# Performance work log

Hardware: AMD Instinct MI355X
Metric: run time of the kernel (lower is better)

## Reference

```python
import jax, jax.numpy as jnp
import numpy as np

NUM_HEADS = 16
THETA = 10000.0


def _rope(x, pos, theta):
    # x: [b, h, s, d_k] with d_k even; rotate interleaved pairs (even, odd)
    d = x.shape[-1]
    inv_freq = theta ** (-jnp.arange(0, d, 2, dtype=jnp.float32) / d)  # [d/2]
    ang = pos.astype(jnp.float32)[:, None] * inv_freq                  # [s, d/2]
    cos = jnp.cos(ang)[None, None]                                     # [1,1,s,d/2]
    sin = jnp.sin(ang)[None, None]
    x1 = x[..., 0::2]
    x2 = x[..., 1::2]
    r1 = x1 * cos - x2 * sin
    r2 = x1 * sin + x2 * cos
    return jnp.stack([r1, r2], axis=-1).reshape(x.shape)


def setup_inputs() -> dict:
    key = jax.random.key(0)
    ks = jax.random.split(key, 5)
    B, S, D = 2, 2048, 1024
    x = jax.random.normal(ks[0], (B, S, D), dtype=jnp.float32)
    scale = 0.02
    Wq = jax.random.normal(ks[1], (D, D), dtype=jnp.float32) * scale
    Wk = jax.random.normal(ks[2], (D, D), dtype=jnp.float32) * scale
    Wv = jax.random.normal(ks[3], (D, D), dtype=jnp.float32) * scale
    Wo = jax.random.normal(ks[4], (D, D), dtype=jnp.float32) * scale
    return {"x": x, "Wq": Wq, "Wk": Wk, "Wv": Wv, "Wo": Wo}


def reference(x, Wq, Wk, Wv, Wo):
    B, S, D = x.shape
    H = NUM_HEADS
    dk = D // H
    # QKV projections (bias-free Linear: y = x @ W^T, W is [out, in])
    q = (x @ Wq.T).reshape(B, S, H, dk).transpose(0, 2, 1, 3)  # [b,h,s,dk]
    k = (x @ Wk.T).reshape(B, S, H, dk).transpose(0, 2, 1, 3)
    v = (x @ Wv.T).reshape(B, S, H, dk).transpose(0, 2, 1, 3)
    pos = jnp.arange(S)
    q = _rope(q, pos, THETA)
    k = _rope(k, pos, THETA)
    # naive masked SDPA, causal mask
    scores = jnp.einsum('bhqd,bhkd->bhqk', q, k) / (dk ** 0.5)
    causal = jnp.tril(jnp.ones((S, S), dtype=bool))
    scores = jnp.where(causal, scores, -jnp.inf)
    attn = jax.nn.softmax(scores, axis=-1)
    out = jnp.einsum('bhqk,bhkd->bhqd', attn, v)
    out = out.transpose(0, 2, 1, 3).reshape(B, S, D)
    return out @ Wo.T
```

## Files before the change

### kernel.cpp

```cpp
#include <hip/hip_runtime.h>
#include <hip/hip_bf16.h>
#include <stdint.h>

typedef __bf16 bf16;
typedef __bf16 bf16x8 __attribute__((ext_vector_type(8)));
typedef float f32x4 __attribute__((ext_vector_type(4)));
typedef float f32x16 __attribute__((ext_vector_type(16)));

#define B_ 2
#define S_ 2048
#define D_ 1024
#define H_ 16
#define DK 64
#define M_ 4096

__device__ __forceinline__ void gload_lds16(const void* g, void* l) {
  __builtin_amdgcn_global_load_lds(
      (const __attribute__((address_space(1))) uint32_t*)(uintptr_t)g,
      (__attribute__((address_space(3))) uint32_t*)(uintptr_t)l, 16, 0, 0);
}

__device__ __forceinline__ uint32_t pkbf(float a, float b) {
  union { uint32_t u; struct { bf16 x, y; } s; } r;
  r.s.x = (bf16)a; r.s.y = (bf16)b;
  return r.u;
}

struct alignas(8) B4s { bf16 a, b, c, d; };

__global__ __launch_bounds__(256) void cvt_all_kernel(
    const float* __restrict__ x, const float* __restrict__ wq, const float* __restrict__ wk,
    const float* __restrict__ wv, const float* __restrict__ wo,
    bf16* __restrict__ xb, bf16* __restrict__ wqb, bf16* __restrict__ wkb,
    bf16* __restrict__ wvb, bf16* __restrict__ wob) {
  int i = blockIdx.x * 256 + threadIdx.x;
  const float* src;
  bf16* dst;
  int off;
  if (i < 1048576) { src = x; dst = xb; off = i; }
  else if (i < 1310720) { src = wq; dst = wqb; off = i - 1048576; }
  else if (i < 1572864) { src = wk; dst = wkb; off = i - 1310720; }
  else if (i < 1835008) { src = wv; dst = wvb; off = i - 1572864; }
  else { src = wo; dst = wob; off = i - 1835008; }
  float4 v = reinterpret_cast<const float4*>(src)[off];
  B4s o{(bf16)v.x, (bf16)v.y, (bf16)v.z, (bf16)v.w};
  reinterpret_cast<B4s*>(dst)[off] = o;
}

template <int MODE>
__global__ __launch_bounds__(256, 3) void gemm_kernel(
    const bf16* __restrict__ A,
    const bf16* __restrict__ W0, const bf16* __restrict__ W1, const bf16* __restrict__ W2,
    bf16* __restrict__ q_out, bf16* __restrict__ k_out, bf16* __restrict__ v_out,
    float* __restrict__ c_out) {
  constexpr int BK = 64;
  constexpr int BM = (MODE == 0) ? 128 : 64;
  constexpr int BNR = (MODE == 0) ? 128 : 64;
  constexpr int AM = (MODE == 0) ? 2 : 1;
  constexpr int BN = (MODE == 0) ? 2 : 1;
  constexpr int NT = (MODE == 0) ? 24 : 16;
  constexpr int PERX = (MODE == 0) ? 96 : 128;
  __shared__ bf16 Alds[BM * BK];
  __shared__ bf16 Blds[BNR * BK];
  const int tid = threadIdx.x;
  const int w = tid >> 6, l = tid & 63;
  const int l31 = l & 31, hh = l >> 5;
  const int lin = (blockIdx.x & 7) * PERX + (blockIdx.x >> 3);
  const int m0 = (lin / NT) * BM;
  const int nt = lin % NT;
  const bf16* W;
  int n0;
  const int rt = (MODE == 0) ? (nt >> 3) : 0;
  if (MODE == 0) {
    W = rt == 0 ? W0 : (rt == 1 ? W1 : W2);
    n0 = (nt & 7) * 128;
  } else {
    W = W0;
    n0 = nt * 64;
  }
  const int K = 1024;
  const int wm = (MODE == 0) ? (w >> 1) * 64 : (w & 1) * 32;
  const int wn = (MODE == 0) ? (w & 1) * 64 : (w >> 1) * 32;
  const int srow = w * 8 + (l >> 3);
  const int scol = ((l & 7) * 8) ^ (((l >> 3) & 7) * 8);
  const int swz = (l & 7) * 8;
  f32x16 acc[AM][BN] = {};
  for (int k0 = 0; k0 < K; k0 += BK) {
    const bf16* Ab = A + (size_t)m0 * K + k0;
    const bf16* Bb = W + (size_t)n0 * K + k0;
#pragma unroll
    for (int c = 0; c < BM / 32; ++c)
      gload_lds16(Ab + (size_t)(c * 32 + srow) * K + scol, Alds + (c * 32 + w * 8) * BK);
#pragma unroll
    for (int c = 0; c < BNR / 32; ++c)
      gload_lds16(Bb + (size_t)(c * 32 + srow) * K + scol, Blds + (c * 32 + w * 8) * BK);
    __syncthreads();
    bf16x8 af[AM][4], bfr[BN][4];
#pragma unroll
    for (int am = 0; am < AM; ++am)
#pragma unroll
      for (int t = 0; t < 4; ++t)
        af[am][t] = *reinterpret_cast<const bf16x8*>(
            Alds + (wm + am * 32 + l31) * BK + ((t * 16 + hh * 8) ^ swz));
#pragma unroll
    for (int bn = 0; bn < BN; ++bn)
#pragma unroll
      for (int t = 0; t < 4; ++t)
        bfr[bn][t] = *reinterpret_cast<const bf16x8*>(
            Blds + (wn + bn * 32 + l31) * BK + ((t * 16 + hh * 8) ^ swz));
#pragma unroll
    for (int t = 0; t < 4; ++t)
#pragma unroll
      for (int am = 0; am < AM; ++am)
#pragma unroll
        for (int bn = 0; bn < BN; ++bn)
          acc[am][bn] = __builtin_amdgcn_mfma_f32_32x32x16_bf16(af[am][t], bfr[bn][t],
                                                               acc[am][bn], 0, 0, 0);
    __syncthreads();
  }
#pragma unroll
  for (int am = 0; am < AM; ++am)
#pragma unroll
    for (int bn = 0; bn < BN; ++bn)
#pragma unroll
      for (int r = 0; r < 16; ++r) {
        int m = m0 + wm + am * 32 + (r & 3) + 8 * (r >> 2) + 4 * hh;
        int n = n0 + wn + bn * 32 + l31;
        float v = acc[am][bn][r];
        if (MODE == 0) {
          bf16* dst = rt == 0 ? q_out : (rt == 1 ? k_out : v_out);
          int h = n >> 6, d = n & 63;
          int b = m >> 11, s = m & 2047;
          dst[(((size_t)b * H_ + h) * S_ + s) * DK + d] = (bf16)v;
        } else {
          c_out[(size_t)m * D_ + n] = v;
        }
      }
}

__global__ __launch_bounds__(256) void rope_kernel(bf16* __restrict__ Q, bf16* __restrict__ K) {
  const int NG = 32 * 2048 * 8;
  int idx = blockIdx.x * 256 + threadIdx.x;
  bf16* X = Q;
  float sc = 0.18033688f;
  if (idx >= NG) { X = K; idx -= NG; sc = 1.0f; }
  int g = idx & 7;
  int s = (idx >> 3) & 2047;
  int bh = idx >> 14;
  size_t off = ((size_t)bh * S_ + s) * DK + g * 8;
  bf16x8 v = *reinterpret_cast<const bf16x8*>(X + off);
  bf16x8 o;
  const float c0 = -0.4152410118609203f;
  float fs = (float)s;
#pragma unroll
  for (int p = 0; p < 4; ++p) {
    int i = g * 4 + p;
    float ang = fs * exp2f((float)i * c0);
    float sn = __sinf(ang), cs = __cosf(ang);
    float x1 = (float)v[2 * p], x2 = (float)v[2 * p + 1];
    o[2 * p]     = (bf16)((x1 * cs - x2 * sn) * sc);
    o[2 * p + 1] = (bf16)((x1 * sn + x2 * cs) * sc);
  }
  *reinterpret_cast<bf16x8*>(X + off) = o;
}

__global__ __launch_bounds__(256, 4) void attn_kernel(
    const bf16* __restrict__ Q, const bf16* __restrict__ K, const bf16* __restrict__ V,
    bf16* __restrict__ O) {
  __shared__ __align__(16) char smem[40960];
  bf16* K3 = (bf16*)smem;
  bf16* Vt2 = (bf16*)smem + 12288;
  float* MG = (float*)smem;
  const int tid = threadIdx.x;
  const int w = tid >> 6, l = tid & 63;
  const int ql = l & 31, h = l >> 5;
  const int kh = w >> 1, qh = w & 1;
  const int bid = blockIdx.x;
  const int u = (bid >> 5) & 7;
  const int j = bid >> 8;
  const int qt = (j == 0) ? u : (j == 1) ? 31 - u : (j == 2) ? u + 8 : 23 - u;
  const int bh = bid & 31;
  const size_t base = (size_t)bh * S_ * DK;

  const size_t qrow = base + (size_t)(qt * 64 + qh * 32 + ql) * DK;
  bf16x8 qf[4];
#pragma unroll
  for (int t = 0; t < 4; ++t)
    qf[t] = *reinterpret_cast<const bf16x8*>(Q + qrow + t * 16 + h * 8);

  float l_run = 0.f;
  f32x16 o0 = {}, o1 = {};

  auto stageK = [&](int kt, int buf) {
#pragma unroll
    for (int c = 0; c < 2; ++c) {
      int row = c * 32 + w * 8 + (l >> 3);
      int col = ((l & 7) * 8) ^ ((row & 7) * 8);
      gload_lds16(K + base + (size_t)(kt * 64 + row) * DK + col,
                  K3 + buf * 4096 + c * 2048 + w * 512);
    }
  };
  auto loadV = [&](int kt, bf16x8 (&pv)[2]) {
    const bf16* vp = V + base + (size_t)(kt * 64 + l) * DK + w * 16;
    pv[0] = *reinterpret_cast<const bf16x8*>(vp);
    pv[1] = *reinterpret_cast<const bf16x8*>(vp + 8);
  };
  auto writeV = [&](int vb, const bf16x8 (&pv)[2]) {
    bf16* Vt = Vt2 + vb * 4096;
#pragma unroll
    for (int j2 = 0; j2 < 8; ++j2) {
      Vt[(w * 16 + j2) * 64 + (l ^ (j2 * 8))] = pv[0][j2];
      Vt[(w * 16 + 8 + j2) * 64 + (l ^ (j2 * 8))] = pv[1][j2];
    }
  };

  {
    bf16x8 pv[2];
    loadV(0, pv);
    stageK(0, 0);
    if (qt >= 1) stageK(1, 1);
    writeV(0, pv);
    if (qt >= 1) {
      asm volatile("s_waitcnt vmcnt(2)" ::: "memory");
    } else {
      asm volatile("s_waitcnt vmcnt(0)" ::: "memory");
    }
    asm volatile("s_waitcnt lgkmcnt(0)" ::: "memory");
    __builtin_amdgcn_sched_barrier(0);
    __builtin_amdgcn_s_barrier();
    __builtin_amdgcn_sched_barrier(0);
  }

  const int swzd = (ql & 7) * 8;
  const int keyA = kh * 32 + ql;
  const int limq = qh * 32 + ql;
  bf16x8 pvv[2];
  int kb = 0, kb2 = 2;

  for (int kt = 0; kt <= qt; ++kt) {
    const int vb = kt & 1;
    const bool pre = kt < qt;
    const bool pre2 = kt + 2 <= qt;
    const bool lastt = (kt == qt);
    const bool skipw = lastt && (kh == 1) && (qh == 0);
    if (pre) loadV(kt + 1, pvv);
    if (pre2) stageK(kt + 2, kb2);
    if (!skipw) {
      f32x16 ss = {};
      __builtin_amdgcn_s_setprio(1);
#pragma unroll
      for (int t = 0; t < 4; ++t) {
        bf16x8 kf = *reinterpret_cast<const bf16x8*>(
            K3 + kb * 4096 + keyA * 64 + ((t * 16 + h * 8) ^ ((keyA & 7) * 8)));
        ss = __builtin_amdgcn_mfma_f32_32x32x16_bf16(kf, qf[t], ss, 0, 0, 0);
      }
      __builtin_amdgcn_s_setprio(0);
      if (lastt) {
#pragma unroll
        for (int r = 0; r < 16; ++r) {
          int kl = kh * 32 + (r & 3) + 8 * (r >> 2) + 4 * h;
          if (kl > limq) ss[r] = -INFINITY;
        }
      }
      float t0 = 0.f, t1 = 0.f, t2 = 0.f, t3 = 0.f;
#pragma unroll
      for (int r = 0; r < 16; r += 4) {
        float p0 = exp2f(ss[r]);
        float p1 = exp2f(ss[r + 1]);
        float p2 = exp2f(ss[r + 2]);
        float p3 = exp2f(ss[r + 3]);
        ss[r] = p0; ss[r + 1] = p1; ss[r + 2] = p2; ss[r + 3] = p3;
        t0 += p0; t1 += p1; t2 += p2; t3 += p3;
      }
      l_run += (t0 + t1) + (t2 + t3);
      uint32_t Wq_[4][2];
#pragma unroll
      for (int g = 0; g < 4; ++g) {
        Wq_[g][0] = pkbf(ss[4 * g + 0], ss[4 * g + 1]);
        Wq_[g][1] = pkbf(ss[4 * g + 2], ss[4 * g + 3]);
      }
      __builtin_amdgcn_s_setprio(1);
#pragma unroll
      for (int ks = 0; ks < 2; ++ks) {
        uint32_t a0 = Wq_[2 * ks][0], a1 = Wq_[2 * ks][1];
        uint32_t b0 = Wq_[2 * ks + 1][0], b1 = Wq_[2 * ks + 1][1];
        uint32_t sxa0 = (uint32_t)__shfl_xor((int)a0, 32);
        uint32_t sxa1 = (uint32_t)__shfl_xor((int)a1, 32);
        uint32_t sxb0 = (uint32_t)__shfl_xor((int)b0, 32);
        uint32_t sxb1 = (uint32_t)__shfl_xor((int)b1, 32);
        union { uint32_t u[4]; bf16x8 v; } pa;
        pa.u[0] = h ? sxb0 : a0;
        pa.u[1] = h ? sxb1 : a1;
        pa.u[2] = h ? b0 : sxa0;
        pa.u[3] = h ? b1 : sxa1;
        int col = (kh * 32 + ks * 16 + h * 8) ^ swzd;
        const bf16* Vt = Vt2 + vb * 4096;
        bf16x8 v0 = *reinterpret_cast<const bf16x8*>(&Vt[ql * 64 + col]);
        bf16x8 v1 = *reinterpret_cast<const bf16x8*>(&Vt[(32 + ql) * 64 + col]);
        o0 = __builtin_amdgcn_mfma_f32_32x32x16_bf16(pa.v, v0, o0, 0, 0, 0);
        o1 = __builtin_amdgcn_mfma_f32_32x32x16_bf16(pa.v, v1, o1, 0, 0, 0);
      }
      __builtin_amdgcn_s_setprio(0);
    }
    if (pre) writeV(vb ^ 1, pvv);
    asm volatile("s_waitcnt vmcnt(2)" ::: "memory");
    asm volatile("s_waitcnt lgkmcnt(0)" ::: "memory");
    __builtin_amdgcn_sched_barrier(0);
    __builtin_amdgcn_s_barrier();
    __builtin_amdgcn_sched_barrier(0);
    kb = (kb == 2) ? 0 : kb + 1;
    kb2 = (kb2 == 2) ? 0 : kb2 + 1;
  }

  l_run += __shfl_xor(l_run, 32);
  __syncthreads();
  if (kh == 1) {
    int off = (qh * 64 + l) * 33;
    MG[off] = l_run;
#pragma unroll
    for (int r = 0; r < 16; ++r) {
      MG[off + 1 + r] = o0[r];
      MG[off + 17 + r] = o1[r];
    }
  }
  __syncthreads();
  if (kh == 0) {
    int off = (qh * 64 + l) * 33;
    float inv = 1.0f / (l_run + MG[off]);
    const int b = bh >> 4, hd = bh & 15;
#pragma unroll
    for (int r = 0; r < 16; ++r) {
      int rowl = (r & 3) + 8 * (r >> 2) + 4 * h;
      float invr = __shfl(inv, rowl);
      int qr = qt * 64 + qh * 32 + rowl;
      size_t ooff = ((size_t)b * S_ + qr) * D_ + hd * 64;
      O[ooff + ql] = (bf16)((o0[r] + MG[off + 1 + r]) * invr);
      O[ooff + 32 + ql] = (bf16)((o1[r] + MG[off + 17 + r]) * invr);
    }
  }
}

extern "C" void kernel_launch(void* const* d_in, const int* in_sizes, int n_in,
                              void* d_out, int out_size, void* d_ws, size_t ws_size,
                              hipStream_t stream) {
  const float* x  = (const float*)d_in[0];
  const float* Wq = (const float*)d_in[1];
  const float* Wk = (const float*)d_in[2];
  const float* Wv = (const float*)d_in[3];
  const float* Wo = (const float*)d_in[4];
  float* out = (float*)d_out;
  char* ws = (char*)d_ws;

  bf16* xb  = (bf16*)(ws + ((size_t)0 << 20));
  bf16* wqb = (bf16*)(ws + ((size_t)8 << 20));
  bf16* wkb = (bf16*)(ws + ((size_t)10 << 20));
  bf16* wvb = (bf16*)(ws + ((size_t)12 << 20));
  bf16* wob = (bf16*)(ws + ((size_t)14 << 20));
  bf16* Qb  = (bf16*)(ws + ((size_t)16 << 20));
  bf16* Kb  = (bf16*)(ws + ((size_t)24 << 20));
  bf16* Vb  = (bf16*)(ws + ((size_t)32 << 20));
  bf16* Ob  = (bf16*)(ws + ((size_t)40 << 20));

  cvt_all_kernel<<<8192, 256, 0, stream>>>(x, Wq, Wk, Wv, Wo, xb, wqb, wkb, wvb, wob);
  gemm_kernel<0><<<768, 256, 0, stream>>>(xb, wqb, wkb, wvb, Qb, Kb, Vb, nullptr);
  rope_kernel<<<4096, 256, 0, stream>>>(Qb, Kb);
  attn_kernel<<<1024, 256, 0, stream>>>(Qb, Kb, Vb, Ob);
  gemm_kernel<1><<<1024, 256, 0, stream>>>(Ob, wob, nullptr, nullptr, nullptr, nullptr,
                                           nullptr, out);
}
```

Baseline: 105.2 us.

## Triple-buffer GEMM LDS staging with BK=32 and async prefetch two tiles ahead

Restructures the projection GEMM main loop from a single-buffered load-sync-compute pattern into a three-stage LDS ring that prefetches tiles two k-steps ahead using global_load_lds. Manual vmcnt waits and a single barrier per step replace the two __syncthreads. The K tile is halved to 32 to keep LDS use bounded, with a matching new swizzle. The goal is to hide global memory latency behind MFMA work, at the cost of more loop iterations and hand-written waitcnt logic that must be exactly right.

```diff
diff --git a/kernel.cpp b/kernel.cpp
--- a/kernel.cpp
+++ b/kernel.cpp
@@ -53,15 +53,21 @@
     const bf16* __restrict__ W0, const bf16* __restrict__ W1, const bf16* __restrict__ W2,
     bf16* __restrict__ q_out, bf16* __restrict__ k_out, bf16* __restrict__ v_out,
     float* __restrict__ c_out) {
-  constexpr int BK = 64;
+  constexpr int BK = 32;
   constexpr int BM = (MODE == 0) ? 128 : 64;
   constexpr int BNR = (MODE == 0) ? 128 : 64;
   constexpr int AM = (MODE == 0) ? 2 : 1;
   constexpr int BN = (MODE == 0) ? 2 : 1;
   constexpr int NT = (MODE == 0) ? 24 : 16;
   constexpr int PERX = (MODE == 0) ? 96 : 128;
-  __shared__ bf16 Alds[BM * BK];
-  __shared__ bf16 Blds[BNR * BK];
+  constexpr int AE = BM * BK;
+  constexpr int BE = BNR * BK;
+  constexpr int ACALLS = BM / 64;
+  constexpr int BCALLS = BNR / 64;
+  constexpr int INF = ACALLS + BCALLS;
+  __shared__ bf16 smem[3 * (AE + BE)];
+  bf16* Ab3 = smem;
+  bf16* Bb3 = smem + 3 * AE;
   const int tid = threadIdx.x;
   const int w = tid >> 6, l = tid & 63;
   const int l31 = l & 31, hh = l >> 5;
@@ -81,43 +87,73 @@
   const int K = 1024;
   const int wm = (MODE == 0) ? (w >> 1) * 64 : (w & 1) * 32;
   const int wn = (MODE == 0) ? (w & 1) * 64 : (w >> 1) * 32;
-  const int srow = w * 8 + (l >> 3);
-  const int scol = ((l & 7) * 8) ^ (((l >> 3) & 7) * 8);
-  const int swz = (l & 7) * 8;
+  const int sr = l >> 2;
+  const int sc = ((l & 3) * 8) ^ ((sr & 3) * 8);
+  const int rswz = (l31 & 3) * 8;
+
+  auto stage = [&](int kt, int buf) {
+    const bf16* Ag = A + (size_t)m0 * K + kt * BK;
+    const bf16* Bg = W + (size_t)n0 * K + kt * BK;
+#pragma unroll
+    for (int c = 0; c < ACALLS; ++c)
+      gload_lds16(Ag + (size_t)(c * 64 + w * 16 + sr) * K + sc,
+                  Ab3 + buf * AE + (c * 64 + w * 16) * BK);
+#pragma unroll
+    for (int c = 0; c < BCALLS; ++c)
+      gload_lds16(Bg + (size_t)(c * 64 + w * 16 + sr) * K + sc,
+                  Bb3 + buf * BE + (c * 64 + w * 16) * BK);
+  };
+
   f32x16 acc[AM][BN] = {};
-  for (int k0 = 0; k0 < K; k0 += BK) {
-    const bf16* Ab = A + (size_t)m0 * K + k0;
-    const bf16* Bb = W + (size_t)n0 * K + k0;
-#pragma unroll
-    for (int c = 0; c < BM / 32; ++c)
-      gload_lds16(Ab + (size_t)(c * 32 + srow) * K + scol, Alds + (c * 32 + w * 8) * BK);
-#pragma unroll
-    for (int c = 0; c < BNR / 32; ++c)
-      gload_lds16(Bb + (size_t)(c * 32 + srow) * K + scol, Blds + (c * 32 + w * 8) * BK);
-    __syncthreads();
-    bf16x8 af[AM][4], bfr[BN][4];
+  stage(0, 0);
+  stage(1, 1);
+  if constexpr (INF == 4) asm volatile("s_waitcnt vmcnt(4)" ::: "memory");
+  else                    asm volatile("s_waitcnt vmcnt(2)" ::: "memory");
+  __builtin_amdgcn_sched_barrier(0);
+  __builtin_amdgcn_s_barrier();
+  __builtin_amdgcn_sched_barrier(0);
+
+  int kb = 0, kb2 = 2;
+  for (int k = 0; k < 32; ++k) {
+    const bool pre = (k + 2 < 32);
+    if (pre) stage(k + 2, kb2);
+    bf16x8 af[AM][2], bfr[BN][2];
 #pragma unroll
     for (int am = 0; am < AM; ++am)
 #pragma unroll
-      for (int t = 0; t < 4; ++t)
+      for (int t = 0; t < 2; ++t)
         af[am][t] = *reinterpret_cast<const bf16x8*>(
-            Alds + (wm + am * 32 + l31) * BK + ((t * 16 + hh * 8) ^ swz));
+            Ab3 + kb * AE + (wm + am * 32 + l31) * BK + ((t * 16 + hh * 8) ^ rswz));
 #pragma unroll
     for (int bn = 0; bn < BN; ++bn)
 #pragma unroll
-      for (int t = 0; t < 4; ++t)
+      for (int t = 0; t < 2; ++t)
         bfr[bn][t] = *reinterpret_cast<const bf16x8*>(
-            Blds + (wn + bn * 32 + l31) * BK + ((t * 16 + hh * 8) ^ swz));
-#pragma unroll
-    for (int t = 0; t < 4; ++t)
+            Bb3 + kb * BE + (wn + bn * 32 + l31) * BK + ((t * 16 + hh * 8) ^ rswz));
+#pragma unroll
+    for (int t = 0; t < 2; ++t)
 #pragma unroll
       for (int am = 0; am < AM; ++am)
 #pragma unroll
         for (int bn = 0; bn < BN; ++bn)
           acc[am][bn] = __builtin_amdgcn_mfma_f32_32x32x16_bf16(af[am][t], bfr[bn][t],
                                                                acc[am][bn], 0, 0, 0);
-    __syncthreads();
-  }
+    if (k < 31) {
+      if (pre) {
+        if constexpr (INF == 4) asm volatile("s_waitcnt vmcnt(4)" ::: "memory");
+        else                    asm volatile("s_waitcnt vmcnt(2)" ::: "memory");
+      } else {
+        asm volatile("s_waitcnt vmcnt(0)" ::: "memory");
+      }
+      asm volatile("s_waitcnt lgkmcnt(0)" ::: "memory");
+      __builtin_amdgcn_sched_barrier(0);
+      __builtin_amdgcn_s_barrier();
+      __builtin_amdgcn_sched_barrier(0);
+    }
+    kb = (kb == 2) ? 0 : kb + 1;
+    kb2 = (kb2 == 2) ? 0 : kb2 + 1;
+  }
+
 #pragma unroll
   for (int am = 0; am < AM; ++am)
 #pragma unroll
```

Measured after the change: 114.8 us. 1.09x slower.
